# Performance work log

Hardware: AMD Instinct MI355X
Metric: run time of the kernel (lower is better)

Reference implementation:

```python
import jax, jax.numpy as jnp
import numpy as np


def conv2d(x, w, b, pad):
    # NCHW conv, stride 1, symmetric padding
    out = jax.lax.conv_general_dilated(
        x, w, window_strides=(1, 1), padding=[(pad, pad), (pad, pad)],
        dimension_numbers=("NCHW", "OIHW", "NCHW"))
    return out + b[None, :, None, None]


def setup_inputs() -> dict:
    key = jax.random.key(0)
    ks = jax.random.split(key, 18)
    B, C, H, W = 4, 256, 64, 64
    Cq = C // 16  # 16
    Ck = C // 8   # 32
    s = 0.02
    return {
        "x": jax.random.normal(ks[0], (B, C, H, W), jnp.float32),
        "dw1_w": jax.random.normal(ks[1], (Cq, C, 7, 7), jnp.float32) * s,
        "dw1_b": jnp.zeros((Cq,), jnp.float32),
        "dw2_w": jax.random.normal(ks[2], (Cq, C, 11, 11), jnp.float32) * s,
        "dw2_b": jnp.zeros((Cq,), jnp.float32),
        "key_w": jax.random.normal(ks[3], (Ck, C, 1, 1), jnp.float32) * s,
        "key_b": jnp.zeros((Ck,), jnp.float32),
        "value_w": jax.random.normal(ks[4], (C, C, 1, 1), jnp.float32) * s,
        "value_b": jnp.zeros((C,), jnp.float32),
        "conv1_w": jax.random.normal(ks[5], (Cq, C, 3, 3), jnp.float32) * s,
        "conv1_b": jnp.zeros((Cq,), jnp.float32),
        "conv2_w": jax.random.normal(ks[6], (C, Cq, 3, 3), jnp.float32) * s,
        "conv2_b": jnp.zeros((C,), jnp.float32),
        "se_w": jax.random.normal(ks[7], (C, C, 1, 1), jnp.float32) * s,
        "se_b": jnp.zeros((C,), jnp.float32),
        "gamma1": jnp.zeros((1,), jnp.float32) + 0.1,  # nonzero so attention path is exercised
        "gamma2": jnp.zeros((1,), jnp.float32) + 0.1,
    }


def reference(x, dw1_w, dw1_b, dw2_w, dw2_b, key_w, key_b, value_w, value_b,
              conv1_w, conv1_b, conv2_w, conv2_b, se_w, se_b, gamma1, gamma2):
    B, C, H, W = x.shape
    HW = H * W
    # q: concat of 7x7 and 11x11 conv branches -> (B, HW, C//8)
    q = jnp.concatenate([conv2d(x, dw1_w, dw1_b, 3), conv2d(x, dw2_w, dw2_b, 5)], axis=1)
    q = q.reshape(B, -1, HW).transpose(0, 2, 1)
    # k: 1x1 conv -> (B, C//8, HW)
    k = conv2d(x, key_w, key_b, 0).reshape(B, -1, HW)
    # raw (unscaled) full spatial attention, softmax over last dim
    att = jax.nn.softmax(jnp.einsum("bnc,bcm->bnm", q, k), axis=-1)  # (B, HW, HW)
    v = conv2d(x, value_w, value_b, 0).reshape(B, C, HW)
    out = jnp.einsum("bcm,bnm->bcn", v, att).reshape(B, C, H, W)
    # local conv branch + channel attention (SE)
    y = conv2d(jax.nn.silu(conv2d(x, conv1_w, conv1_b, 1)), conv2_w, conv2_b, 1)
    pooled = jnp.mean(y, axis=(2, 3), keepdims=True)  # (B, C, 1, 1)
    se = y * jax.nn.sigmoid(conv2d(pooled, se_w, se_b, 0))
    return gamma1 * out + gamma2 * se + x
```

## Files before the change

### kernel.cpp

```cpp
#include <hip/hip_runtime.h>

typedef unsigned short u16;
typedef unsigned u32;
typedef __bf16 bf16x8 __attribute__((ext_vector_type(8)));
typedef float f32x4 __attribute__((ext_vector_type(4)));
typedef float f32x16 __attribute__((ext_vector_type(16)));

#define MFMA16(A,B,C) __builtin_amdgcn_mfma_f32_16x16x32_bf16((A),(B),(C),0,0,0)
#define MFMA32(A,B,C) __builtin_amdgcn_mfma_f32_32x32x16_bf16((A),(B),(C),0,0,0)

__device__ __forceinline__ u16 f2b(float f){
  union { float f; unsigned u; } X; X.f = f;
  unsigned r = X.u + 0x7FFFu + ((X.u >> 16) & 1u);
  return (u16)(r >> 16);
}
__device__ __forceinline__ float b2f(u16 h){
  union { unsigned u; float f; } X; X.u = ((unsigned)h) << 16; return X.f;
}
__device__ __forceinline__ bf16x8 ld_frag(const u16* p){
  union { uint4 u; bf16x8 v; } U; U.u = *(const uint4*)p; return U.v;
}
__device__ __forceinline__ u32 pkbf(float a, float b){
  u32 r; asm("v_cvt_pk_bf16_f32 %0, %1, %2" : "=v"(r) : "v"(a), "v"(b)); return r;
}
__device__ __forceinline__ void pl32swap(u32& x, u32& y){
  auto r = __builtin_amdgcn_permlane32_swap(x, y, false, false);
  x = r[0]; y = r[1];
}
__device__ __forceinline__ void gld16(const u16* g, u16* l){
  __builtin_amdgcn_global_load_lds(
      (const __attribute__((address_space(1))) u32*)g,
      (__attribute__((address_space(3))) u32*)l, 16, 0, 0);
}

__global__ __launch_bounds__(256) void k_prep_w(
    const float* __restrict__ dw1, const float* __restrict__ dw2,
    const float* __restrict__ cw1, const float* __restrict__ kw,
    const float* __restrict__ vw,  const float* __restrict__ cw2,
    u16* __restrict__ wB, u16* __restrict__ wC,
    u16* __restrict__ kwt, u16* __restrict__ vwt, u16* __restrict__ w2t){
  int i = blockIdx.x * 256 + threadIdx.x;
  const int NB = 991232, NC = 73728, NK = 8192, NV = 65536, N2 = 40960;
  if(i < NB){
    int tap = i >> 13, rem = i & 8191;
    int chunk = rem >> 9, r2 = rem & 511;
    int oc = r2 >> 4, ci = chunk*16 + (r2 & 15);
    int dy = tap / 11, dx = tap - dy*11;
    float v;
    if(oc < 16){
      v = (dy >= 2 && dy <= 8 && dx >= 2 && dx <= 8) ? dw1[(oc*256 + ci)*49 + (dy-2)*7 + (dx-2)] : 0.f;
    } else {
      v = dw2[((oc-16)*256 + ci)*121 + tap];
    }
    wB[i] = f2b(v);
    return;
  }
  i -= NB;
  if(i < NC){
    int tap = i >> 13, rem = i & 8191;
    int chunk = rem >> 9, r2 = rem & 511;
    int oc = r2 >> 4, ci = chunk*16 + (r2 & 15);
    wC[i] = (oc < 16) ? f2b(cw1[(oc*256 + ci)*9 + tap]) : (u16)0;
    return;
  }
  i -= NC;
  if(i < NK){ kwt[i] = f2b(kw[i]); return; }
  i -= NK;
  if(i < NV){ vwt[i] = f2b(vw[i]); return; }
  i -= NV;
  if(i < N2){
    int co = i/160, kk = i - co*160;
    int tap = kk >> 4, ci = kk & 15;
    w2t[i] = (tap < 9) ? f2b(cw2[co*144 + ci*9 + tap]) : (u16)0;
    return;
  }
}

__global__ __launch_bounds__(256) void k_prep_x(const float* __restrict__ x, u16* __restrict__ xp){
  __shared__ float tile[32][33];
  const int bid = blockIdx.x;
  const int b = bid >> 10, rem = bid & 1023;
  const int c0 = (rem >> 7) << 5, m0 = (rem & 127) << 5;
  const int t = threadIdx.x;
  { const int cg = t >> 5, mm = t & 31;
    #pragma unroll
    for(int i=0;i<4;i++)
      tile[cg*4+i][mm] = x[((size_t)(b*256 + c0 + cg*4 + i) << 12) + m0 + mm];
  }
  __syncthreads();
  { const int cp = (t & 15) << 1, mloc = t >> 4;
    #pragma unroll
    for(int half = 0; half < 2; ++half){
      const int ml = half*16 + mloc;
      const int m = m0 + ml;
      const int yy = (m >> 6) + 5, xx = (m & 63) + 5;
      const int ci = c0 + cp;
      const int chunk = ci >> 4, wi = ci & 15;
      u16 lo = f2b(tile[cp][ml]), hi = f2b(tile[cp+1][ml]);
      *(unsigned*)&xp[(((size_t)(b*16 + chunk)*74 + yy)*80 + xx)*16 + wi] = ((unsigned)hi << 16) | lo;
    }
  }
}

__global__ __launch_bounds__(256, 2) void k_qconv(
    const u16* __restrict__ xp, const u16* __restrict__ wB, const u16* __restrict__ wC,
    u16* __restrict__ qp){
  __shared__ __align__(16) u16 buf[17920];
  const int bid = blockIdx.x;
  const int rg = bid & 15, b = (bid >> 4) & 3, kq = bid >> 6;
  const int y0 = rg << 2;
  const int t = threadIdx.x, wv = t >> 6, lane = t & 63;
  const int m = lane & 31, kh = lane >> 5;
  const int laneoff = m*16 + kh*8;
  const f32x16 z16 = {0.f,0.f,0.f,0.f,0.f,0.f,0.f,0.f,0.f,0.f,0.f,0.f,0.f,0.f,0.f,0.f};
  f32x16 accA = z16, accB = z16, acc1A = z16, acc1B = z16;

  #pragma unroll 1
  for(int c = 0; c < 2; ++c){
    const int chunk = kq*2 + c;
    const uint4* src = (const uint4*)(xp + ((size_t)((b*16 + chunk)*74 + y0))*1280);
    __syncthreads();
    for(int e = t; e < 2240; e += 256){
      ((uint4*)buf)[(e & 1)*1120 + (e >> 1)] = src[e];
    }
    __syncthreads();
    const u16* wBc = wB + chunk*512 + laneoff;
    const u16* wCc = wC + chunk*512 + laneoff;
    const u16* ap = buf + kh*8960 + (wv*80 + m)*8;
    bf16x8 Brow[2][11];
    #pragma unroll
    for(int dx = 0; dx < 11; ++dx) Brow[0][dx] = ld_frag(wBc + dx*8192);
    #pragma unroll
    for(int dy = 0; dy < 11; ++dy){
      if(dy < 10){
        const u16* wnext = wBc + (dy+1)*11*8192;
        #pragma unroll
        for(int dx = 0; dx < 11; ++dx) Brow[(dy+1)&1][dx] = ld_frag(wnext + dx*8192);
      }
      const u16* rowp = ap + dy*640;
      #pragma unroll
      for(int dx = 0; dx < 11; ++dx){
        bf16x8 B = Brow[dy&1][dx];
        bf16x8 A0 = ld_frag(rowp + dx*8);
        bf16x8 A1 = ld_frag(rowp + dx*8 + 256);
        accA = MFMA32(A0, B, accA);
        accB = MFMA32(A1, B, accB);
        if(dy >= 4 && dy <= 6 && dx >= 4 && dx <= 6){
          bf16x8 B1 = ld_frag(wCc + ((dy-4)*3 + (dx-4))*8192);
          acc1A = MFMA32(A0, B1, acc1A);
          acc1B = MFMA32(A1, B1, acc1B);
        }
      }
    }
  }

  u16* qb = qp + ((size_t)kq*16384 + (b << 12) + (y0 + wv)*64) * 48;
  #pragma unroll
  for(int reg = 0; reg < 16; ++reg){
    const int row = (reg & 3) + ((reg >> 2) << 3) + (kh << 2);
    qb[row*48 + m] = f2b(accA[reg]);
    qb[(32 + row)*48 + m] = f2b(accB[reg]);
    if(m < 16){
      qb[row*48 + 32 + m] = f2b(acc1A[reg]);
      qb[(32 + row)*48 + 32 + m] = f2b(acc1B[reg]);
    }
  }
}

__global__ __launch_bounds__(256) void k_qfin(
    const u16* __restrict__ qp, const float* __restrict__ b7,
    const float* __restrict__ b11, const float* __restrict__ b1,
    u16* __restrict__ q_t, u16* __restrict__ t1){
  const int t = threadIdx.x, wv = t >> 6, lane = t & 63;
  const int px = blockIdx.x*4 + wv;
  if(lane >= 48) return;
  const size_t off = (size_t)px*48 + lane;
  float s = 0.f;
  #pragma unroll
  for(int sp = 0; sp < 8; ++sp) s += b2f(qp[off + (size_t)sp*786432]);
  const float LOG2E = 1.44269504f;
  if(lane < 16){
    q_t[px*32 + lane] = f2b((s + b7[lane]) * LOG2E);
  } else if(lane < 32){
    q_t[px*32 + lane] = f2b((s + b11[lane - 16]) * LOG2E);
  } else {
    float v = s + b1[lane - 32];
    t1[px*16 + lane - 32] = f2b(v / (1.f + __expf(-v)));
  }
}

__global__ __launch_bounds__(256) void k_kv(
    const u16* __restrict__ xp, const u16* __restrict__ vwt, const u16* __restrict__ kwt,
    const float* __restrict__ vb, const float* __restrict__ kb,
    u16* __restrict__ vt, u16* __restrict__ k_t){
  const int bid = blockIdx.x;
  const int h = bid & 3, blk = (bid >> 2) & 63, b = bid >> 8;
  const int wv = threadIdx.x >> 6, lane = threadIdx.x & 63;
  const int col = lane & 15, quad = lane >> 4;
  const int m0 = (blk << 6) + (wv << 4);
  f32x4 z = {0.f,0.f,0.f,0.f};
  f32x4 av[4], ak[2];
  #pragma unroll
  for(int i=0;i<4;i++) av[i] = z;
  ak[0] = z; ak[1] = z;
  const int m = m0 + col;
  const int py = (m >> 6) + 5, pxx = (m & 63) + 5;
  #pragma unroll 1
  for(int ch = 0; ch < 8; ++ch){
    const int cio = ch*32 + quad*8;
    const int chunk = cio >> 4, wi = cio & 15;
    bf16x8 xf = ld_frag(xp + (((size_t)(b*16 + chunk)*74 + py)*80 + pxx)*16 + wi);
    #pragma unroll
    for(int ct2 = 0; ct2 < 4; ++ct2){
      bf16x8 wf = ld_frag(vwt + (((h*4 + ct2)*16 + col) << 8) + cio);
      av[ct2] = MFMA16(wf, xf, av[ct2]);
    }
    if(h == 0){
      #pragma unroll
      for(int kt = 0; kt < 2; ++kt){
        bf16x8 kf = ld_frag(kwt + ((kt*16 + col) << 8) + cio);
        ak[kt] = MFMA16(xf, kf, ak[kt]);
      }
    }
  }
  const size_t kgb = ((size_t)(b*256 + (m0 >> 4)));
  const int hi2 = col >> 3, j = col & 7;
  #pragma unroll
  for(int ct2 = 0; ct2 < 4; ++ct2){
    #pragma unroll
    for(int r = 0; r < 4; ++r){
      const int c = (h*4 + ct2)*16 + quad*4 + r;
      vt[((((kgb*8 + (c >> 5))*2 + hi2)*32) + (c & 31))*8 + j] = f2b(av[ct2][r] + vb[c]);
    }
  }
  if(h == 0){
    #pragma unroll
    for(int kt = 0; kt < 2; ++kt){
      #pragma unroll
      for(int r = 0; r < 4; ++r){
        const int mq = b*4096 + m0 + quad*4 + r;
        k_t[mq*32 + kt*16 + col] = f2b((ak[kt][r] + kb[kt*16 + col]) );
      }
    }
  }
}

__global__ __launch_bounds__(256, 2) void k_attn(
    const u16* __restrict__ q_t, const u16* __restrict__ k_t,
    const u16* __restrict__ vt, u16* __restrict__ Op,
    float* __restrict__ lsav){
  __shared__ __align__(16) u16 V[2][16384];
  const int bid = blockIdx.x;
  const int q0 = (bid & 31) << 7, b = (bid >> 5) & 3, ks = bid >> 7;
  const int t = threadIdx.x, wv = t >> 6, lane = t & 63;
  const int cq = lane & 31, hi = lane >> 5;

  const u16* qrow = q_t + ((size_t)(b*4096 + q0 + wv*32 + cq) << 5) + hi*8;
  const bf16x8 qf0 = ld_frag(qrow), qf1 = ld_frag(qrow + 16);
  const u16* kbase = k_t + ((size_t)(b*4096 + ks*1024 + cq) << 5) + hi*8;
  const u16* vsrc = vt + ((size_t)(b*256 + ks*64) << 12);

  const f32x16 z16 = {0.f,0.f,0.f,0.f,0.f,0.f,0.f,0.f,0.f,0.f,0.f,0.f,0.f,0.f,0.f,0.f};
  f32x16 acc[8];
  #pragma unroll
  for(int i=0;i<8;i++) acc[i] = z16;
  float lp0=0.f, lp1=0.f, lp2=0.f, lp3=0.f;

  #pragma unroll
  for(int s = 0; s < 8; ++s)
    gld16(vsrc + (size_t)(s*256 + t)*8, &V[0][(s*256 + (wv << 6))*8]);
  __builtin_amdgcn_sched_barrier(0);
  bf16x8 kc0 = ld_frag(kbase),        kc1 = ld_frag(kbase + 16);
  bf16x8 kc2 = ld_frag(kbase + 1024), kc3 = ld_frag(kbase + 1040);

  #pragma unroll 1
  for(int it = 0; it < 16; ++it){
    const int cur = it & 1;
    asm volatile("s_waitcnt vmcnt(4)" ::: "memory");
    __builtin_amdgcn_s_barrier();
    __builtin_amdgcn_sched_barrier(0);
    const bf16x8 ka0 = kc0, ka1 = kc1, ka2 = kc2, ka3 = kc3;
    if(it < 15){
      const u16* gb = vsrc + ((size_t)(it + 1) << 14);
      #pragma unroll
      for(int s = 0; s < 8; ++s)
        gld16(gb + (size_t)(s*256 + t)*8, &V[cur ^ 1][(s*256 + (wv << 6))*8]);
      __builtin_amdgcn_sched_barrier(0);
      const u16* kpn = kbase + ((size_t)(it + 1) << 11);
      kc0 = ld_frag(kpn);        kc1 = ld_frag(kpn + 16);
      kc2 = ld_frag(kpn + 1024); kc3 = ld_frag(kpn + 1040);
    }
    const u16* Vb = &V[cur][hi*256 + cq*8];
    #pragma unroll
    for(int sub = 0; sub < 2; ++sub){
      const bf16x8 kf0 = sub ? ka2 : ka0;
      const bf16x8 kf1 = sub ? ka3 : ka1;
      f32x16 S = MFMA32(kf0, qf0, z16);
      S = MFMA32(kf1, qf1, S);
      float p[16];
      #pragma unroll
      for(int rr = 0; rr < 16; ++rr) p[rr] = exp2f(S[rr]);
      #pragma unroll
      for(int rr = 0; rr < 16; rr += 4){
        lp0 += p[rr]; lp1 += p[rr+1]; lp2 += p[rr+2]; lp3 += p[rr+3];
      }
      u32 a0 = pkbf(p[0], p[1]),   b0 = pkbf(p[4], p[5]);
      u32 a1 = pkbf(p[2], p[3]),   b1 = pkbf(p[6], p[7]);
      u32 c0 = pkbf(p[8], p[9]),   d0 = pkbf(p[12], p[13]);
      u32 c1 = pkbf(p[10], p[11]), d1 = pkbf(p[14], p[15]);
      pl32swap(a0, b0); pl32swap(a1, b1); pl32swap(c0, d0); pl32swap(c1, d1);
      union { u32 w[4]; bf16x8 v; } A0, A1;
      A0.w[0] = a0; A0.w[1] = a1; A0.w[2] = b0; A0.w[3] = b1;
      A1.w[0] = c0; A1.w[1] = c1; A1.w[2] = d0; A1.w[3] = d1;
      const u16* f0 = Vb + sub*8192;
      #pragma unroll
      for(int ct = 0; ct < 8; ++ct){
        acc[ct] = MFMA32(A0.v, ld_frag(f0 + ct*512),        acc[ct]);
        acc[ct] = MFMA32(A1.v, ld_frag(f0 + 4096 + ct*512), acc[ct]);
      }
    }
  }

  float lt = lp0 + lp1 + lp2 + lp3;
  lt += __shfl_xor(lt, 32);
  if(lane < 32)
    lsav[ks*16384 + b*4096 + q0 + wv*32 + cq] = lt;
  const float invl = 1.f / lt;
  u16* ob = Op + (((size_t)(ks*16384 + b*4096 + q0 + wv*32)) << 8) + cq;
  #pragma unroll
  for(int reg = 0; reg < 16; ++reg){
    const int row = (reg & 3) + ((reg >> 2) << 3) + (hi << 2);
    const float inv = __shfl(invl, row);
    u16* orow = ob + ((size_t)row << 8);
    #pragma unroll
    for(int ct = 0; ct < 8; ++ct)
      orow[ct*32] = f2b(acc[ct][reg] * inv);
  }
}

__global__ __launch_bounds__(256) void k_conv2(
    const u16* __restrict__ t1, const u16* __restrict__ w2t, const float* __restrict__ b2,
    u16* __restrict__ y_t, float* __restrict__ pooled){
  __shared__ __align__(16) u16 im[64][168];
  __shared__ float pool_l[64];
  const int bid = blockIdx.x;
  const int h = bid & 3, y = (bid >> 2) & 63, b = bid >> 8;
  const int t = threadIdx.x;
  if(t < 64) pool_l[t] = 0.f;
  const u16* t1b = t1 + ((size_t)(b*4096) << 4);
  { const int px = t >> 2, ci0 = (t & 3) << 2;
    #pragma unroll
    for(int tap = 0; tap < 9; ++tap){
      const int ky = (tap*11) >> 5, kx = tap - ky*3;
      const int ryy = y + ky - 1, rxx = px + kx - 1;
      uint2 val = make_uint2(0u, 0u);
      if((unsigned)ryy < 64u && (unsigned)rxx < 64u)
        val = *(const uint2*)(t1b + (((ryy << 6) + rxx) << 4) + ci0);
      *(uint2*)&im[px][tap*16 + ci0] = val;
    }
    for(int e = t; e < 1024; e += 256){ im[e >> 4][144 + (e & 15)] = 0; }
  }
  __syncthreads();
  const int wv = t >> 6, lane = t & 63, col = lane & 15, quad = lane >> 4;
  const f32x4 z = {0.f,0.f,0.f,0.f};
  f32x4 acc[4];
  #pragma unroll
  for(int i=0;i<4;i++) acc[i] = z;
  #pragma unroll
  for(int ch = 0; ch < 5; ++ch){
    bf16x8 af = ld_frag(&im[wv*16 + col][ch*32 + quad*8]);
    #pragma unroll
    for(int j = 0; j < 4; ++j){
      bf16x8 wf = ld_frag(w2t + ((h*4 + j)*16 + col)*160 + ch*32 + quad*8);
      acc[j] = MFMA16(af, wf, acc[j]);
    }
  }
  const int m0 = (y << 6) + (wv << 4) + (quad << 2);
  #pragma unroll
  for(int j = 0; j < 4; ++j){
    const int c = (h*4 + j)*16 + col;
    const float bias = b2[c];
    float s = 0.f;
    #pragma unroll
    for(int r = 0; r < 4; ++r){
      float v = acc[j][r] + bias;
      y_t[((size_t)(b*4096 + m0 + r) << 8) + c] = f2b(v);
      s += v;
    }
    s += __shfl_xor(s, 16); s += __shfl_xor(s, 32);
    if(quad == 0) atomicAdd(&pool_l[c - h*64], s);
  }
  __syncthreads();
  if(t < 64) atomicAdd(&pooled[b*256 + h*64 + t], pool_l[t]);
}

__global__ __launch_bounds__(256) void k_final(
    const u16* __restrict__ Op, const u16* __restrict__ y_t, const float* __restrict__ x,
    const float* __restrict__ lsav, const float* __restrict__ pooled,
    const float* __restrict__ sew, const float* __restrict__ seb,
    const float* __restrict__ g1p, const float* __restrict__ g2p,
    float* __restrict__ out){
  __shared__ float tO[32][65];
  __shared__ float tY[32][65];
  __shared__ float gate_l[32];
  const int bid = blockIdx.x;
  const int b = bid >> 9, rem = bid & 511;
  const int c0 = (rem >> 6) << 5, m0 = (rem & 63) << 6;
  const int t = threadIdx.x;
  const float g1 = g1p[0], g2 = g2p[0];
  { const int cl = t >> 3, k0 = (t & 7) << 5;
    const int c = c0 + cl;
    const float* wr = sew + (size_t)c*256 + k0;
    const float* pr = pooled + b*256 + k0;
    float part = 0.f;
    #pragma unroll
    for(int j = 0; j < 32; j += 4){
      float4 w4 = *(const float4*)(wr + j);
      float4 p4 = *(const float4*)(pr + j);
      part += w4.x*p4.x + w4.y*p4.y + w4.z*p4.z + w4.w*p4.w;
    }
    part += __shfl_xor(part, 1); part += __shfl_xor(part, 2); part += __shfl_xor(part, 4);
    if((t & 7) == 0){
      float a = part * (1.f/4096.f) + seb[c];
      gate_l[cl] = g2 / (1.f + __expf(-a));
    }
  }
  { const int ml = t >> 2, cg = (t & 3) << 3;
    const int gq = b*4096 + m0 + ml;
    const float l0 = lsav[gq], l1 = lsav[16384 + gq], l2 = lsav[32768 + gq], l3 = lsav[49152 + gq];
    const float inv = 1.f / (l0 + l1 + l2 + l3);
    const float w0 = l0*inv, w1 = l1*inv, w2 = l2*inv, w3 = l3*inv;
    const size_t base = ((size_t)gq << 8) + c0 + cg;
    union { uint4 u; u16 s[8]; } A0, A1, A2, A3;
    A0.u = *(const uint4*)(Op + base);
    A1.u = *(const uint4*)(Op + base + ((size_t)16384 << 8));
    A2.u = *(const uint4*)(Op + base + ((size_t)32768 << 8));
    A3.u = *(const uint4*)(Op + base + ((size_t)49152 << 8));
    #pragma unroll
    for(int i = 0; i < 8; ++i)
      tO[cg+i][ml] = w0*b2f(A0.s[i]) + w1*b2f(A1.s[i]) + w2*b2f(A2.s[i]) + w3*b2f(A3.s[i]);
    const u16* yrow = y_t + base;
    uint4 yu = *(const uint4*)yrow;
    tY[cg+0][ml]=b2f((u16)(yu.x & 0xffffu)); tY[cg+1][ml]=b2f((u16)(yu.x >> 16));
    tY[cg+2][ml]=b2f((u16)(yu.y & 0xffffu)); tY[cg+3][ml]=b2f((u16)(yu.y >> 16));
    tY[cg+4][ml]=b2f((u16)(yu.z & 0xffffu)); tY[cg+5][ml]=b2f((u16)(yu.z >> 16));
    tY[cg+6][ml]=b2f((u16)(yu.w & 0xffffu)); tY[cg+7][ml]=b2f((u16)(yu.w >> 16));
  }
  __syncthreads();
  { const int cl = t >> 3, mg = (t & 7) << 3;
    const int c = c0 + cl;
    const float gate = gate_l[cl];
    const float* xrow = x + ((size_t)(b*256 + c) << 12) + m0 + mg;
    float* orow = out + ((size_t)(b*256 + c) << 12) + m0 + mg;
    float4 x0 = *(const float4*)xrow, x1 = *(const float4*)(xrow + 4);
    float4 r0, r1;
    r0.x = g1*tO[cl][mg+0] + gate*tY[cl][mg+0] + x0.x;
    r0.y = g1*tO[cl][mg+1] + gate*tY[cl][mg+1] + x0.y;
    r0.z = g1*tO[cl][mg+2] + gate*tY[cl][mg+2] + x0.z;
    r0.w = g1*tO[cl][mg+3] + gate*tY[cl][mg+3] + x0.w;
    r1.x = g1*tO[cl][mg+4] + gate*tY[cl][mg+4] + x1.x;
    r1.y = g1*tO[cl][mg+5] + gate*tY[cl][mg+5] + x1.y;
    r1.z = g1*tO[cl][mg+6] + gate*tY[cl][mg+6] + x1.z;
    r1.w = g1*tO[cl][mg+7] + gate*tY[cl][mg+7] + x1.w;
    *(float4*)orow = r0;
    *(float4*)(orow + 4) = r1;
  }
}

extern "C" void kernel_launch(void* const* d_in, const int* in_sizes, int n_in,
                              void* d_out, int out_size, void* d_ws, size_t ws_size,
                              hipStream_t stream){
  (void)in_sizes; (void)n_in; (void)out_size; (void)ws_size;
  const float* x    = (const float*)d_in[0];
  const float* dw1w = (const float*)d_in[1];
  const float* dw1b = (const float*)d_in[2];
  const float* dw2w = (const float*)d_in[3];
  const float* dw2b = (const float*)d_in[4];
  const float* keyw = (const float*)d_in[5];
  const float* keyb = (const float*)d_in[6];
  const float* valw = (const float*)d_in[7];
  const float* valb = (const float*)d_in[8];
  const float* c1w  = (const float*)d_in[9];
  const float* c1b  = (const float*)d_in[10];
  const float* c2w  = (const float*)d_in[11];
  const float* c2b  = (const float*)d_in[12];
  const float* sew  = (const float*)d_in[13];
  const float* seb  = (const float*)d_in[14];
  const float* g1   = (const float*)d_in[15];
  const float* g2   = (const float*)d_in[16];
  float* out = (float*)d_out;

  char* w = (char*)d_ws;
  auto take = [&](size_t bytes) -> char* {
    char* p = w; w += (bytes + 255) & ~(size_t)255; return p;
  };
  u16*  Op   = (u16*)  take(33554432);
  u16*  q_t  = (u16*)  take(1048576);
  u16*  k_t  = (u16*)  take(1048576);
  u16*  vt   = (u16*)  take(8388608);
  u16*  t1   = (u16*)  take(524288);
  u16*  y_t  = (u16*)  take(8388608);
  u16*  kwt  = (u16*)  take(16384);
  u16*  vwt  = (u16*)  take(131072);
  u16*  w2t  = (u16*)  take(81920);
  float* pooled = (float*)take(4096);
  float* lsav   = (float*)take(262144);

  u16*  xp = Op;
  u16*  qp = Op + 6062080;
  u16*  wB = vt;
  u16*  wC = vt + 991232;

  hipMemsetAsync(xp, 0, 12124160, stream);
  hipMemsetAsync(pooled, 0, 4096, stream);
  k_prep_w<<<4608, 256, 0, stream>>>(dw1w, dw2w, c1w, keyw, valw, c2w, wB, wC, kwt, vwt, w2t);
  k_prep_x<<<4096, 256, 0, stream>>>(x, xp);
  k_qconv<<<512, 256, 0, stream>>>(xp, wB, wC, qp);
  k_qfin<<<4096, 256, 0, stream>>>(qp, dw1b, dw2b, c1b, q_t, t1);
  k_kv<<<1024, 256, 0, stream>>>(xp, vwt, kwt, valb, keyb, vt, k_t);
  k_attn<<<512, 256, 0, stream>>>(q_t, k_t, vt, Op, lsav);
  k_conv2<<<1024, 256, 0, stream>>>(t1, w2t, c2b, y_t, pooled);
  k_final<<<2048, 256, 0, stream>>>(Op, y_t, x, lsav, pooled, sew, seb, g1, g2, out);
}
```

Measured before the change: 269.4 us.

## Merge independent kernels into combined launches to overlap stages

Three pairs of independent kernels are merged into single launches that dispatch on block index: the weight and input prep, q-conv with k/v projection, and attention with the second local conv. This removes launch gaps and lets the short kernels fill the tail of the long ones on the device. The weight scratch moves from the v buffer to the y buffer so the merged kv blocks can write v without overwriting weights still being read. The merged kernels share the larger shared-memory allocation and the stricter launch bounds, which may lower occupancy for the formerly lighter kernels.

```diff
diff --git a/kernel.cpp b/kernel.cpp
--- a/kernel.cpp
+++ b/kernel.cpp
@@ -33,13 +33,12 @@
       (__attribute__((address_space(3))) u32*)l, 16, 0, 0);
 }
 
-__global__ __launch_bounds__(256) void k_prep_w(
+__device__ __forceinline__ void prep_w_body(int i,
     const float* __restrict__ dw1, const float* __restrict__ dw2,
     const float* __restrict__ cw1, const float* __restrict__ kw,
     const float* __restrict__ vw,  const float* __restrict__ cw2,
     u16* __restrict__ wB, u16* __restrict__ wC,
     u16* __restrict__ kwt, u16* __restrict__ vwt, u16* __restrict__ w2t){
-  int i = blockIdx.x * 256 + threadIdx.x;
   const int NB = 991232, NC = 73728, NK = 8192, NV = 65536, N2 = 40960;
   if(i < NB){
     int tap = i >> 13, rem = i & 8191;
@@ -76,16 +75,14 @@
   }
 }
 
-__global__ __launch_bounds__(256) void k_prep_x(const float* __restrict__ x, u16* __restrict__ xp){
-  __shared__ float tile[32][33];
-  const int bid = blockIdx.x;
+__device__ __forceinline__ void prep_x_body(int bid, int t, float* tile ,
+    const float* __restrict__ x, u16* __restrict__ xp){
   const int b = bid >> 10, rem = bid & 1023;
   const int c0 = (rem >> 7) << 5, m0 = (rem & 127) << 5;
-  const int t = threadIdx.x;
   { const int cg = t >> 5, mm = t & 31;
     #pragma unroll
     for(int i=0;i<4;i++)
-      tile[cg*4+i][mm] = x[((size_t)(b*256 + c0 + cg*4 + i) << 12) + m0 + mm];
+      tile[(cg*4+i)*33 + mm] = x[((size_t)(b*256 + c0 + cg*4 + i) << 12) + m0 + mm];
   }
   __syncthreads();
   { const int cp = (t & 15) << 1, mloc = t >> 4;
@@ -96,20 +93,34 @@
       const int yy = (m >> 6) + 5, xx = (m & 63) + 5;
       const int ci = c0 + cp;
       const int chunk = ci >> 4, wi = ci & 15;
-      u16 lo = f2b(tile[cp][ml]), hi = f2b(tile[cp+1][ml]);
+      u16 lo = f2b(tile[cp*33 + ml]), hi = f2b(tile[(cp+1)*33 + ml]);
       *(unsigned*)&xp[(((size_t)(b*16 + chunk)*74 + yy)*80 + xx)*16 + wi] = ((unsigned)hi << 16) | lo;
     }
   }
 }
 
-__global__ __launch_bounds__(256, 2) void k_qconv(
+__global__ __launch_bounds__(256) void k_prep(
+    const float* __restrict__ x, u16* __restrict__ xp,
+    const float* __restrict__ dw1, const float* __restrict__ dw2,
+    const float* __restrict__ cw1, const float* __restrict__ kw,
+    const float* __restrict__ vw,  const float* __restrict__ cw2,
+    u16* __restrict__ wB, u16* __restrict__ wC,
+    u16* __restrict__ kwt, u16* __restrict__ vwt, u16* __restrict__ w2t){
+  __shared__ float tile[32*33];
+  const int bid = blockIdx.x;
+  if(bid < 4096){
+    prep_x_body(bid, threadIdx.x, tile, x, xp);
+  } else {
+    prep_w_body((bid - 4096)*256 + threadIdx.x, dw1, dw2, cw1, kw, vw, cw2, wB, wC, kwt, vwt, w2t);
+  }
+}
+
+__device__ __forceinline__ void qconv_body(int bid, int t, u16* buf ,
     const u16* __restrict__ xp, const u16* __restrict__ wB, const u16* __restrict__ wC,
     u16* __restrict__ qp){
-  __shared__ __align__(16) u16 buf[17920];
-  const int bid = blockIdx.x;
   const int rg = bid & 15, b = (bid >> 4) & 3, kq = bid >> 6;
   const int y0 = rg << 2;
-  const int t = threadIdx.x, wv = t >> 6, lane = t & 63;
+  const int wv = t >> 6, lane = t & 63;
   const int m = lane & 31, kh = lane >> 5;
   const int laneoff = m*16 + kh*8;
   const f32x16 z16 = {0.f,0.f,0.f,0.f,0.f,0.f,0.f,0.f,0.f,0.f,0.f,0.f,0.f,0.f,0.f,0.f};
@@ -167,6 +178,73 @@
   }
 }
 
+__device__ __forceinline__ void kv_body(int bid, int tid,
+    const u16* __restrict__ xp, const u16* __restrict__ vwt, const u16* __restrict__ kwt,
+    const float* __restrict__ vb, const float* __restrict__ kb,
+    u16* __restrict__ vt, u16* __restrict__ k_t){
+  const int h = bid & 3, blk = (bid >> 2) & 63, b = bid >> 8;
+  const int wv = tid >> 6, lane = tid & 63;
+  const int col = lane & 15, quad = lane >> 4;
+  const int m0 = (blk << 6) + (wv << 4);
+  f32x4 z = {0.f,0.f,0.f,0.f};
+  f32x4 av[4], ak[2];
+  #pragma unroll
+  for(int i=0;i<4;i++) av[i] = z;
+  ak[0] = z; ak[1] = z;
+  const int m = m0 + col;
+  const int py = (m >> 6) + 5, pxx = (m & 63) + 5;
+  #pragma unroll 1
+  for(int ch = 0; ch < 8; ++ch){
+    const int cio = ch*32 + quad*8;
+    const int chunk = cio >> 4, wi = cio & 15;
+    bf16x8 xf = ld_frag(xp + (((size_t)(b*16 + chunk)*74 + py)*80 + pxx)*16 + wi);
+    #pragma unroll
+    for(int ct2 = 0; ct2 < 4; ++ct2){
+      bf16x8 wf = ld_frag(vwt + (((h*4 + ct2)*16 + col) << 8) + cio);
+      av[ct2] = MFMA16(wf, xf, av[ct2]);
+    }
+    if(h == 0){
+      #pragma unroll
+      for(int kt = 0; kt < 2; ++kt){
+        bf16x8 kf = ld_frag(kwt + ((kt*16 + col) << 8) + cio);
+        ak[kt] = MFMA16(xf, kf, ak[kt]);
+      }
+    }
+  }
+  const size_t kgb = ((size_t)(b*256 + (m0 >> 4)));
+  const int hi2 = col >> 3, j = col & 7;
+  #pragma unroll
+  for(int ct2 = 0; ct2 < 4; ++ct2){
+    #pragma unroll
+    for(int r = 0; r < 4; ++r){
+      const int c = (h*4 + ct2)*16 + quad*4 + r;
+      vt[((((kgb*8 + (c >> 5))*2 + hi2)*32) + (c & 31))*8 + j] = f2b(av[ct2][r] + vb[c]);
+    }
+  }
+  if(h == 0){
+    #pragma unroll
+    for(int kt = 0; kt < 2; ++kt){
+      #pragma unroll
+      for(int r = 0; r < 4; ++r){
+        const int mq = b*4096 + m0 + quad*4 + r;
+        k_t[mq*32 + kt*16 + col] = f2b((ak[kt][r] + kb[kt*16 + col]) );
+      }
+    }
+  }
+}
+
+__global__ __launch_bounds__(256, 2) void k_qconv_kv(
+    const u16* __restrict__ xp, const u16* __restrict__ wB, const u16* __restrict__ wC,
+    u16* __restrict__ qp,
+    const u16* __restrict__ vwt, const u16* __restrict__ kwt,
+    const float* __restrict__ vb, const float* __restrict__ kb,
+    u16* __restrict__ vt, u16* __restrict__ k_t){
+  __shared__ __align__(16) u16 buf[17920];
+  const int bid = blockIdx.x;
+  if(bid < 512) qconv_body(bid, threadIdx.x, buf, xp, wB, wC, qp);
+  else          kv_body(bid - 512, threadIdx.x, xp, vwt, kwt, vb, kb, vt, k_t);
+}
+
 __global__ __launch_bounds__(256) void k_qfin(
     const u16* __restrict__ qp, const float* __restrict__ b7,
     const float* __restrict__ b11, const float* __restrict__ b1,
@@ -189,70 +267,12 @@
   }
 }
 
-__global__ __launch_bounds__(256) void k_kv(
-    const u16* __restrict__ xp, const u16* __restrict__ vwt, const u16* __restrict__ kwt,
-    const float* __restrict__ vb, const float* __restrict__ kb,
-    u16* __restrict__ vt, u16* __restrict__ k_t){
-  const int bid = blockIdx.x;
-  const int h = bid & 3, blk = (bid >> 2) & 63, b = bid >> 8;
-  const int wv = threadIdx.x >> 6, lane = threadIdx.x & 63;
-  const int col = lane & 15, quad = lane >> 4;
-  const int m0 = (blk << 6) + (wv << 4);
-  f32x4 z = {0.f,0.f,0.f,0.f};
-  f32x4 av[4], ak[2];
-  #pragma unroll
-  for(int i=0;i<4;i++) av[i] = z;
-  ak[0] = z; ak[1] = z;
-  const int m = m0 + col;
-  const int py = (m >> 6) + 5, pxx = (m & 63) + 5;
-  #pragma unroll 1
-  for(int ch = 0; ch < 8; ++ch){
-    const int cio = ch*32 + quad*8;
-    const int chunk = cio >> 4, wi = cio & 15;
-    bf16x8 xf = ld_frag(xp + (((size_t)(b*16 + chunk)*74 + py)*80 + pxx)*16 + wi);
-    #pragma unroll
-    for(int ct2 = 0; ct2 < 4; ++ct2){
-      bf16x8 wf = ld_frag(vwt + (((h*4 + ct2)*16 + col) << 8) + cio);
-      av[ct2] = MFMA16(wf, xf, av[ct2]);
-    }
-    if(h == 0){
-      #pragma unroll
-      for(int kt = 0; kt < 2; ++kt){
-        bf16x8 kf = ld_frag(kwt + ((kt*16 + col) << 8) + cio);
-        ak[kt] = MFMA16(xf, kf, ak[kt]);
-      }
-    }
-  }
-  const size_t kgb = ((size_t)(b*256 + (m0 >> 4)));
-  const int hi2 = col >> 3, j = col & 7;
-  #pragma unroll
-  for(int ct2 = 0; ct2 < 4; ++ct2){
-    #pragma unroll
-    for(int r = 0; r < 4; ++r){
-      const int c = (h*4 + ct2)*16 + quad*4 + r;
-      vt[((((kgb*8 + (c >> 5))*2 + hi2)*32) + (c & 31))*8 + j] = f2b(av[ct2][r] + vb[c]);
-    }
-  }
-  if(h == 0){
-    #pragma unroll
-    for(int kt = 0; kt < 2; ++kt){
-      #pragma unroll
-      for(int r = 0; r < 4; ++r){
-        const int mq = b*4096 + m0 + quad*4 + r;
-        k_t[mq*32 + kt*16 + col] = f2b((ak[kt][r] + kb[kt*16 + col]) );
-      }
-    }
-  }
-}
-
-__global__ __launch_bounds__(256, 2) void k_attn(
+__device__ __forceinline__ void attn_body(int bid, int t, u16* Vs ,
     const u16* __restrict__ q_t, const u16* __restrict__ k_t,
     const u16* __restrict__ vt, u16* __restrict__ Op,
     float* __restrict__ lsav){
-  __shared__ __align__(16) u16 V[2][16384];
-  const int bid = blockIdx.x;
   const int q0 = (bid & 31) << 7, b = (bid >> 5) & 3, ks = bid >> 7;
-  const int t = threadIdx.x, wv = t >> 6, lane = t & 63;
+  const int wv = t >> 6, lane = t & 63;
   const int cq = lane & 31, hi = lane >> 5;
 
   const u16* qrow = q_t + ((size_t)(b*4096 + q0 + wv*32 + cq) << 5) + hi*8;
@@ -268,7 +288,7 @@
 
   #pragma unroll
   for(int s = 0; s < 8; ++s)
-    gld16(vsrc + (size_t)(s*256 + t)*8, &V[0][(s*256 + (wv << 6))*8]);
+    gld16(vsrc + (size_t)(s*256 + t)*8, Vs + (s*256 + (wv << 6))*8);
   __builtin_amdgcn_sched_barrier(0);
   bf16x8 kc0 = ld_frag(kbase),        kc1 = ld_frag(kbase + 16);
   bf16x8 kc2 = ld_frag(kbase + 1024), kc3 = ld_frag(kbase + 1040);
@@ -284,13 +304,13 @@
       const u16* gb = vsrc + ((size_t)(it + 1) << 14);
       #pragma unroll
       for(int s = 0; s < 8; ++s)
-        gld16(gb + (size_t)(s*256 + t)*8, &V[cur ^ 1][(s*256 + (wv << 6))*8]);
+        gld16(gb + (size_t)(s*256 + t)*8, Vs + (cur ^ 1)*16384 + (s*256 + (wv << 6))*8);
       __builtin_amdgcn_sched_barrier(0);
       const u16* kpn = kbase + ((size_t)(it + 1) << 11);
       kc0 = ld_frag(kpn);        kc1 = ld_frag(kpn + 16);
       kc2 = ld_frag(kpn + 1024); kc3 = ld_frag(kpn + 1040);
     }
-    const u16* Vb = &V[cur][hi*256 + cq*8];
+    const u16* Vb = Vs + cur*16384 + hi*256 + cq*8;
     #pragma unroll
     for(int sub = 0; sub < 2; ++sub){
       const bf16x8 kf0 = sub ? ka2 : ka0;
@@ -338,15 +358,11 @@
   }
 }
 
-__global__ __launch_bounds__(256) void k_conv2(
+__device__ __forceinline__ void conv2_body(int bid, int t, u16* im_s , float* pool_s ,
     const u16* __restrict__ t1, const u16* __restrict__ w2t, const float* __restrict__ b2,
     u16* __restrict__ y_t, float* __restrict__ pooled){
-  __shared__ __align__(16) u16 im[64][168];
-  __shared__ float pool_l[64];
-  const int bid = blockIdx.x;
   const int h = bid & 3, y = (bid >> 2) & 63, b = bid >> 8;
-  const int t = threadIdx.x;
-  if(t < 64) pool_l[t] = 0.f;
+  if(t < 64) pool_s[t] = 0.f;
   const u16* t1b = t1 + ((size_t)(b*4096) << 4);
   { const int px = t >> 2, ci0 = (t & 3) << 2;
     #pragma unroll
@@ -356,9 +372,9 @@
       uint2 val = make_uint2(0u, 0u);
       if((unsigned)ryy < 64u && (unsigned)rxx < 64u)
         val = *(const uint2*)(t1b + (((ryy << 6) + rxx) << 4) + ci0);
-      *(uint2*)&im[px][tap*16 + ci0] = val;
-    }
-    for(int e = t; e < 1024; e += 256){ im[e >> 4][144 + (e & 15)] = 0; }
+      *(uint2*)(im_s + px*168 + tap*16 + ci0) = val;
+    }
+    for(int e = t; e < 1024; e += 256){ im_s[(e >> 4)*168 + 144 + (e & 15)] = 0; }
   }
   __syncthreads();
   const int wv = t >> 6, lane = t & 63, col = lane & 15, quad = lane >> 4;
@@ -368,7 +384,7 @@
   for(int i=0;i<4;i++) acc[i] = z;
   #pragma unroll
   for(int ch = 0; ch < 5; ++ch){
-    bf16x8 af = ld_frag(&im[wv*16 + col][ch*32 + quad*8]);
+    bf16x8 af = ld_frag(im_s + (wv*16 + col)*168 + ch*32 + quad*8);
     #pragma unroll
     for(int j = 0; j < 4; ++j){
       bf16x8 wf = ld_frag(w2t + ((h*4 + j)*16 + col)*160 + ch*32 + quad*8);
@@ -388,10 +404,21 @@
       s += v;
     }
     s += __shfl_xor(s, 16); s += __shfl_xor(s, 32);
-    if(quad == 0) atomicAdd(&pool_l[c - h*64], s);
+    if(quad == 0) atomicAdd(&pool_s[c - h*64], s);
   }
   __syncthreads();
-  if(t < 64) atomicAdd(&pooled[b*256 + h*64 + t], pool_l[t]);
+  if(t < 64) atomicAdd(&pooled[b*256 + h*64 + t], pool_s[t]);
+}
+
+__global__ __launch_bounds__(256, 2) void k_attn_conv2(
+    const u16* __restrict__ q_t, const u16* __restrict__ k_t,
+    const u16* __restrict__ vt, u16* __restrict__ Op, float* __restrict__ lsav,
+    const u16* __restrict__ t1, const u16* __restrict__ w2t, const float* __restrict__ b2,
+    u16* __restrict__ y_t, float* __restrict__ pooled){
+  __shared__ __align__(16) u16 shm[32768];
+  const int bid = blockIdx.x;
+  if(bid < 512) attn_body(bid, threadIdx.x, shm, q_t, k_t, vt, Op, lsav);
+  else          conv2_body(bid - 512, threadIdx.x, shm, (float*)(shm + 10752), t1, w2t, b2, y_t, pooled);
 }
 
 __global__ __launch_bounds__(256) void k_final(
@@ -508,17 +535,14 @@
 
   u16*  xp = Op;
   u16*  qp = Op + 6062080;
-  u16*  wB = vt;
-  u16*  wC = vt + 991232;
+  u16*  wB = y_t;
+  u16*  wC = y_t + 991232;
 
   hipMemsetAsync(xp, 0, 12124160, stream);
   hipMemsetAsync(pooled, 0, 4096, stream);
-  k_prep_w<<<4608, 256, 0, stream>>>(dw1w, dw2w, c1w, keyw, valw, c2w, wB, wC, kwt, vwt, w2t);
-  k_prep_x<<<4096, 256, 0, stream>>>(x, xp);
-  k_qconv<<<512, 256, 0, stream>>>(xp, wB, wC, qp);
+  k_prep<<<8704, 256, 0, stream>>>(x, xp, dw1w, dw2w, c1w, keyw, valw, c2w, wB, wC, kwt, vwt, w2t);
+  k_qconv_kv<<<1536, 256, 0, stream>>>(xp, wB, wC, qp, vwt, kwt, valb, keyb, vt, k_t);
   k_qfin<<<4096, 256, 0, stream>>>(qp, dw1b, dw2b, c1b, q_t, t1);
-  k_kv<<<1024, 256, 0, stream>>>(xp, vwt, kwt, valb, keyb, vt, k_t);
-  k_attn<<<512, 256, 0, stream>>>(q_t, k_t, vt, Op, lsav);
-  k_conv2<<<1024, 256, 0, stream>>>(t1, w2t, c2b, y_t, pooled);
+  k_attn_conv2<<<1536, 256, 0, stream>>>(q_t, k_t, vt, Op, lsav, t1, w2t, c2b, y_t, pooled);
   k_final<<<2048, 256, 0, stream>>>(Op, y_t, x, lsav, pooled, sew, seb, g1, g2, out);
 }
```

Result: faster. 242.5 us (-10.0%).
